# Kernel tuning notes

Hardware: AMD Instinct MI355X
Metric: run time of the kernel (lower is better)

Reference implementation:

```python
import jax, jax.numpy as jnp
import numpy as np

EMB = 64  # hardcoded char embedding / LSTMCell input size in the module


def lstm_cell(x, h, c, Wih, Whh, bih, bhh):
    # torch LSTMCell: gates = x @ Wih.T + bih + h @ Whh.T + bhh, order i,f,g,o
    g = x @ Wih.T + bih + h @ Whh.T + bhh
    i, f, gg, o = jnp.split(g, 4, axis=-1)
    c_new = jax.nn.sigmoid(f) * c + jax.nn.sigmoid(i) * jnp.tanh(gg)
    h_new = jax.nn.sigmoid(o) * jnp.tanh(c_new)
    return h_new, c_new


def setup_inputs() -> dict:
    key = jax.random.key(0)
    ks = jax.random.split(key, 12)
    B, T = 4096, 32
    V, H, O = 256, 512, 64
    s_e = 1.0 / np.sqrt(H)
    inp = {
        "x": jax.random.randint(ks[0], (B, T), 0, V),
        "mask": jnp.ones((B, T), jnp.float32),
        "emb": jax.random.normal(ks[1], (V, EMB), jnp.float32),
        "Wih1": jax.random.uniform(ks[2], (4 * H, EMB), jnp.float32, -s_e, s_e),
        "Whh1": jax.random.uniform(ks[3], (4 * H, H), jnp.float32, -s_e, s_e),
        "bih1": jax.random.uniform(ks[4], (4 * H,), jnp.float32, -s_e, s_e),
        "bhh1": jax.random.uniform(ks[5], (4 * H,), jnp.float32, -s_e, s_e),
        "Wih2": jax.random.uniform(ks[6], (4 * H, EMB), jnp.float32, -s_e, s_e),
        "Whh2": jax.random.uniform(ks[7], (4 * H, H), jnp.float32, -s_e, s_e),
        "bih2": jax.random.uniform(ks[8], (4 * H,), jnp.float32, -s_e, s_e),
        "bhh2": jax.random.uniform(ks[9], (4 * H,), jnp.float32, -s_e, s_e),
        "Wlin": jax.random.uniform(ks[10], (O, 2 * H), jnp.float32, -s_e, s_e),
        "blin": jax.random.uniform(ks[11], (O,), jnp.float32, -s_e, s_e),
    }
    return inp


def reference(x, mask, emb, Wih1, Whh1, bih1, bhh1, Wih2, Whh2, bih2, bhh2, Wlin, blin):
    B, T = x.shape
    H = Whh1.shape[1]
    xe = emb[x].transpose(1, 0, 2)  # [T, B, 64]
    # mask is transposed in the original but never applied; preserved here.

    def step(carry, xs):
        h1, c1, h2, c2 = carry
        x_fwd, x_bwd = xs
        h1, c1 = lstm_cell(x_fwd, h1, c1, Wih1, Whh1, bih1, bhh1)
        h2, c2 = lstm_cell(x_bwd, h2, c2, Wih2, Whh2, bih2, bhh2)
        return (h1, c1, h2, c2), None

    z = jnp.zeros((B, H), xe.dtype)
    (h1, _, h2, _), _ = jax.lax.scan(step, (z, z, z, z), (xe, xe[::-1]))
    # original's transpose/cat/view/transpose is equivalent to feature concat
    h = jnp.concatenate([h1, h2], axis=1)  # [B, 2H]
    return jax.nn.softmax(h @ Wlin.T + blin, axis=1)
```

## Files before the change

### kernel.cpp

```cpp
#include <hip/hip_runtime.h>


typedef __bf16 bf16x8 __attribute__((ext_vector_type(8)));
typedef float  f32x4  __attribute__((ext_vector_type(4)));

constexpr int BATCH = 4096;
constexpr int TSEQ  = 32;
constexpr int HID   = 512;
constexpr int NG    = 2048;
constexpr int VOC   = 256;
constexpr int OUTD  = 64;
constexpr int HBUF  = 64 * BATCH * 8;

__device__ __forceinline__ unsigned short f2bf(float x) {
  unsigned int u = __builtin_bit_cast(unsigned int, x);
  u += 0x7FFFu + ((u >> 16) & 1u);
  return (unsigned short)(u >> 16);
}
__device__ __forceinline__ float bf2f(unsigned short b) {
  unsigned int u = ((unsigned int)b) << 16;
  return __builtin_bit_cast(float, u);
}
__device__ __forceinline__ float fsig(float x) {
  return __fdividef(1.0f, 1.0f + __expf(-x));
}
__device__ __forceinline__ float ftanh(float x) {
  float e = __expf(-2.0f * fabsf(x));
  float t = (1.0f - e) * __fdividef(1.0f, 1.0f + e);
  return copysignf(t, x);
}
__device__ __forceinline__ bf16x8 ld_frag(const unsigned short* p) {
  uint4 v = *(const uint4*)p;
  return __builtin_bit_cast(bf16x8, v);
}
__device__ __forceinline__ void gll16(const void* g, const void* l) {
  __builtin_amdgcn_global_load_lds(
      (const __attribute__((address_space(1))) unsigned int*)g,
      (__attribute__((address_space(3))) unsigned int*)l, 16, 0, 0);
}

__global__ __launch_bounds__(128)
void build_G(const float* __restrict__ emb, const float* __restrict__ Wih,
             const float* __restrict__ bih, const float* __restrict__ bhh,
             float* __restrict__ G) {
  __shared__ float e[64];
  const int v = blockIdx.y;
  const int tid = threadIdx.x;
  if (tid < 64) e[tid] = emb[v * 64 + tid];
  __syncthreads();
  const int n = blockIdx.x * 128 + tid;
  const float4* w4 = (const float4*)&Wih[n * 64];
  float s = bih[n] + bhh[n];
#pragma unroll
  for (int k = 0; k < 16; ++k) {
    float4 wv = w4[k];
    s += wv.x * e[4 * k] + wv.y * e[4 * k + 1] + wv.z * e[4 * k + 2] + wv.w * e[4 * k + 3];
  }
  G[v * NG + n] = s;
}

__global__ __launch_bounds__(256)
void packW(const float* __restrict__ W, unsigned short* __restrict__ hi,
           unsigned short* __restrict__ lo, int kdim, int nch, int total) {
  int p = blockIdx.x * 256 + threadIdx.x;
  if (p >= total) return;
  int lane = p & 63;
  int c = (p >> 6) % nch;
  int f = (p >> 6) / nch;
  int n = f * 16 + (lane & 15);
  int k = c * 32 + (lane >> 4) * 8;
  const float* src = &W[(size_t)n * kdim + k];
  unsigned short* dh = &hi[(size_t)p * 8];
  unsigned short* dl = &lo[(size_t)p * 8];
#pragma unroll
  for (int e = 0; e < 8; ++e) {
    float x = src[e];
    unsigned short h = f2bf(x);
    dh[e] = h;
    dl[e] = f2bf(x - bf2f(h));
  }
}

__global__ __launch_bounds__(256, 4)
void lstm_step(const int* __restrict__ xTok,
               const unsigned short* __restrict__ h1r_hi, const unsigned short* __restrict__ h1r_lo,
               unsigned short* __restrict__ h1w_hi, unsigned short* __restrict__ h1w_lo,
               const unsigned short* __restrict__ h2r_hi, const unsigned short* __restrict__ h2r_lo,
               unsigned short* __restrict__ h2w_hi, unsigned short* __restrict__ h2w_lo,
               float* __restrict__ c1, float* __restrict__ c2,
               const unsigned short* __restrict__ W1_hi, const unsigned short* __restrict__ W1_lo,
               const unsigned short* __restrict__ W2_hi, const unsigned short* __restrict__ W2_lo,
               const float* __restrict__ G1, const float* __restrict__ G2,
               int t) {
  const int tid = threadIdx.x;
  const int bid = blockIdx.x;
  const int cell = (bid >> 2) & 1;
  const int j0   = (((bid & 3) << 1) | ((bid >> 9) & 1)) * 64;
  const int m0   = ((bid >> 3) & 63) * 64;

  const unsigned short* hr_hi = cell ? h2r_hi : h1r_hi;
  const unsigned short* hr_lo = cell ? h2r_lo : h1r_lo;
  unsigned short* hw_hi = cell ? h2w_hi : h1w_hi;
  unsigned short* hw_lo = cell ? h2w_lo : h1w_lo;
  float* cbuf = cell ? c2 : c1;
  const unsigned short* Whi = cell ? W2_hi : W1_hi;
  const unsigned short* Wlo = cell ? W2_lo : W1_lo;
  const float* G = cell ? G2 : G1;
  const int tx = cell ? (TSEQ - 1 - t) : t;

  __shared__ unsigned short ldsA[2][2][8][64][8];
  __shared__ int toks[64];
  if (tid < 64) toks[tid] = xTok[(m0 + tid) * TSEQ + tx];

  const int srow = tid & 63, schk = tid >> 6;
  const unsigned short* ghi = hr_hi + (size_t)schk * 32768 + (size_t)(m0 + srow) * 8;
  const unsigned short* glo = hr_lo + (size_t)schk * 32768 + (size_t)(m0 + srow) * 8;
  char* lbase = ((char*)ldsA) + tid * 16;

  auto stage = [&](int kt, int buf) {
    const size_t go = (size_t)kt * (8 * 32768);
    char* lb = lbase + buf * 16384;
    gll16(ghi + go,             lb);
    gll16(ghi + go + 4 * 32768, lb + 4096);
    gll16(glo + go,             lb + 8192);
    gll16(glo + go + 4 * 32768, lb + 12288);
  };

  stage(0, 0);
  __syncthreads();

  const int lane = tid & 63, hs = tid >> 6;
  const int lg = lane >> 4, ll = lane & 15;

  const int fb = (j0 >> 4) + hs;
  const unsigned short* Bh = Whi + ((size_t)(fb * 16) * 64 + lane) * 8;
  const unsigned short* Bl = Wlo + ((size_t)(fb * 16) * 64 + lane) * 8;

  f32x4 acc[4][4] = {};

#pragma unroll 1
  for (int kt = 0; kt < 8; ++kt) {
    const int cur = kt & 1;
    if (kt < 7) stage(kt + 1, cur ^ 1);
#pragma unroll
    for (int h = 0; h < 2; ++h) {
      const int c = kt * 2 + h;
      bf16x8 bh[4], bl[4];
#pragma unroll
      for (int g = 0; g < 4; ++g) {
        size_t off = ((size_t)(g * 512 + c)) * 512;
        bh[g] = ld_frag(Bh + off);
        bl[g] = ld_frag(Bl + off);
      }
#pragma unroll
      for (int mf = 0; mf < 4; ++mf) {
        const int row = mf * 16 + ll;
        bf16x8 ah = ld_frag(&ldsA[cur][0][h * 4 + lg][row][0]);
        bf16x8 al = ld_frag(&ldsA[cur][1][h * 4 + lg][row][0]);
#pragma unroll
        for (int g = 0; g < 4; ++g) {
          acc[mf][g] = __builtin_amdgcn_mfma_f32_16x16x32_bf16(ah, bh[g], acc[mf][g], 0, 0, 0);
          acc[mf][g] = __builtin_amdgcn_mfma_f32_16x16x32_bf16(al, bh[g], acc[mf][g], 0, 0, 0);
          acc[mf][g] = __builtin_amdgcn_mfma_f32_16x16x32_bf16(ah, bl[g], acc[mf][g], 0, 0, 0);
        }
      }
    }
    __syncthreads();
  }

  const int jcol = j0 + hs * 16 + ll;
#pragma unroll
  for (int mf = 0; mf < 4; ++mf) {
#pragma unroll
    for (int r = 0; r < 4; ++r) {
      int row = mf * 16 + lg * 4 + r;
      int b = m0 + row;
      const float* g4 = &G[(size_t)toks[row] * NG + jcol];
      float pi = acc[mf][0][r] + g4[0];
      float pf = acc[mf][1][r] + g4[512];
      float pg = acc[mf][2][r] + g4[1024];
      float po = acc[mf][3][r] + g4[1536];
      float ig = fsig(pi), fg = fsig(pf), gg = ftanh(pg), og = fsig(po);
      float cold = cbuf[b * HID + jcol];
      float cn = fg * cold + ig * gg;
      cbuf[b * HID + jcol] = cn;
      float hn = og * ftanh(cn);
      unsigned short hh = f2bf(hn);
      unsigned short hl = f2bf(hn - bf2f(hh));
      int hidx = (jcol >> 3) * (BATCH * 8) + b * 8 + (jcol & 7);
      hw_hi[hidx] = hh;
      hw_lo[hidx] = hl;
    }
  }
}

__global__ __launch_bounds__(256)
void final_linsoft(const unsigned short* __restrict__ h1_hi, const unsigned short* __restrict__ h1_lo,
                   const unsigned short* __restrict__ h2_hi, const unsigned short* __restrict__ h2_lo,
                   const unsigned short* __restrict__ WL_hi, const unsigned short* __restrict__ WL_lo,
                   const float* __restrict__ blin, float* __restrict__ out) {
  const int tid = threadIdx.x;
  const int lane = tid & 63;
  const int w = tid >> 6;
  const int lg = lane >> 4, ll = lane & 15;
  const int m0 = blockIdx.x * 64;
  const int arow = m0 + w * 16 + ll;

  f32x4 acc[4] = {};
#pragma unroll 1
  for (int kt = 0; kt < 32; ++kt) {
    const int k0 = kt * 32;
    const unsigned short* ah_ = (k0 < 512) ? h1_hi : h2_hi;
    const unsigned short* al_ = (k0 < 512) ? h1_lo : h2_lo;
    const int kk0 = k0 & 511;
    const int aidx = (kk0 / 8 + lg) * (BATCH * 8) + arow * 8;
    bf16x8 ah = ld_frag(&ah_[aidx]);
    bf16x8 al = ld_frag(&al_[aidx]);
#pragma unroll
    for (int nf = 0; nf < 4; ++nf) {
      size_t boff = (((size_t)nf * 32 + kt) * 64 + lane) * 8;
      bf16x8 bh = ld_frag(&WL_hi[boff]);
      bf16x8 bl = ld_frag(&WL_lo[boff]);
      acc[nf] = __builtin_amdgcn_mfma_f32_16x16x32_bf16(ah, bh, acc[nf], 0, 0, 0);
      acc[nf] = __builtin_amdgcn_mfma_f32_16x16x32_bf16(al, bh, acc[nf], 0, 0, 0);
      acc[nf] = __builtin_amdgcn_mfma_f32_16x16x32_bf16(ah, bl, acc[nf], 0, 0, 0);
    }
  }

  float bl4[4];
#pragma unroll
  for (int nf = 0; nf < 4; ++nf) bl4[nf] = blin[nf * 16 + ll];

#pragma unroll
  for (int r = 0; r < 4; ++r) {
    float z[4];
    float mx = -3.4e38f;
#pragma unroll
    for (int nf = 0; nf < 4; ++nf) { z[nf] = acc[nf][r] + bl4[nf]; mx = fmaxf(mx, z[nf]); }
#pragma unroll
    for (int d = 1; d < 16; d <<= 1) mx = fmaxf(mx, __shfl_xor(mx, d));
    float s = 0.f;
#pragma unroll
    for (int nf = 0; nf < 4; ++nf) { z[nf] = __expf(z[nf] - mx); s += z[nf]; }
#pragma unroll
    for (int d = 1; d < 16; d <<= 1) s += __shfl_xor(s, d);
    float inv = __fdividef(1.0f, s);
    int row = m0 + w * 16 + lg * 4 + r;
#pragma unroll
    for (int nf = 0; nf < 4; ++nf) out[row * OUTD + nf * 16 + ll] = z[nf] * inv;
  }
}

extern "C" void kernel_launch(void* const* d_in, const int* in_sizes, int n_in,
                              void* d_out, int out_size, void* d_ws, size_t ws_size,
                              hipStream_t stream) {
  const int*   x    = (const int*)  d_in[0];
  const float* emb  = (const float*)d_in[2];
  const float* Wih1 = (const float*)d_in[3];
  const float* Whh1 = (const float*)d_in[4];
  const float* bih1 = (const float*)d_in[5];
  const float* bhh1 = (const float*)d_in[6];
  const float* Wih2 = (const float*)d_in[7];
  const float* Whh2 = (const float*)d_in[8];
  const float* bih2 = (const float*)d_in[9];
  const float* bhh2 = (const float*)d_in[10];
  const float* Wlin = (const float*)d_in[11];
  const float* blin = (const float*)d_in[12];
  float* out = (float*)d_out;

  char* p = (char*)d_ws;
  auto alloc = [&](size_t b) { char* r = p; p += (b + 255) & ~(size_t)255; return r; };

  float* G1 = (float*)alloc((size_t)VOC * NG * 4);
  float* G2 = (float*)alloc((size_t)VOC * NG * 4);
  unsigned short* W1_hi = (unsigned short*)alloc((size_t)NG * HID * 2);
  unsigned short* W1_lo = (unsigned short*)alloc((size_t)NG * HID * 2);
  unsigned short* W2_hi = (unsigned short*)alloc((size_t)NG * HID * 2);
  unsigned short* W2_lo = (unsigned short*)alloc((size_t)NG * HID * 2);
  unsigned short* WL_hi = (unsigned short*)alloc((size_t)OUTD * 1024 * 2);
  unsigned short* WL_lo = (unsigned short*)alloc((size_t)OUTD * 1024 * 2);
  unsigned short* h1_hi = (unsigned short*)alloc((size_t)2 * HBUF * 2);
  unsigned short* h1_lo = (unsigned short*)alloc((size_t)2 * HBUF * 2);
  unsigned short* h2_hi = (unsigned short*)alloc((size_t)2 * HBUF * 2);
  unsigned short* h2_lo = (unsigned short*)alloc((size_t)2 * HBUF * 2);
  float* c1 = (float*)alloc((size_t)BATCH * HID * 4);
  float* c2 = (float*)alloc((size_t)BATCH * HID * 4);

  if ((size_t)(p - (char*)d_ws) > ws_size) return;

  hipMemsetAsync(h1_hi, 0, (size_t)HBUF * 2, stream);
  hipMemsetAsync(h1_lo, 0, (size_t)HBUF * 2, stream);
  hipMemsetAsync(h2_hi, 0, (size_t)HBUF * 2, stream);
  hipMemsetAsync(h2_lo, 0, (size_t)HBUF * 2, stream);
  hipMemsetAsync(c1, 0, (size_t)BATCH * HID * 4, stream);
  hipMemsetAsync(c2, 0, (size_t)BATCH * HID * 4, stream);

  packW<<<dim3(512), 256, 0, stream>>>(Whh1, W1_hi, W1_lo, HID, 16, NG * HID / 8);
  packW<<<dim3(512), 256, 0, stream>>>(Whh2, W2_hi, W2_lo, HID, 16, NG * HID / 8);
  packW<<<dim3(32), 256, 0, stream>>>(Wlin, WL_hi, WL_lo, 1024, 32, OUTD * 1024 / 8);
  build_G<<<dim3(16, VOC), 128, 0, stream>>>(emb, Wih1, bih1, bhh1, G1);
  build_G<<<dim3(16, VOC), 128, 0, stream>>>(emb, Wih2, bih2, bhh2, G2);

  for (int t = 0; t < TSEQ; ++t) {
    int rb = t & 1, wb = rb ^ 1;
    lstm_step<<<dim3(1024), 256, 0, stream>>>(x,
        h1_hi + (size_t)rb * HBUF, h1_lo + (size_t)rb * HBUF,
        h1_hi + (size_t)wb * HBUF, h1_lo + (size_t)wb * HBUF,
        h2_hi + (size_t)rb * HBUF, h2_lo + (size_t)rb * HBUF,
        h2_hi + (size_t)wb * HBUF, h2_lo + (size_t)wb * HBUF,
        c1, c2, W1_hi, W1_lo, W2_hi, W2_lo, G1, G2, t);
  }
  final_linsoft<<<dim3(64), 256, 0, stream>>>(h1_hi, h1_lo, h2_hi, h2_lo,
                                              WL_hi, WL_lo, blin, out);
}
```

Baseline: 1.994 ms.

## Switch LSTM step GEMM to 32x32x16 MFMA with repacked recurrent weights

The recurrent-weight GEMM in each LSTM step now uses 32x32x16 bf16 MFMA instructions instead of 16x16x32. Waves are rearranged into a 2x2 grid of 32-row by 32-column tiles, and a new packing kernel lays out Whh in the matching fragment order. The aim is fewer instructions and better operand reuse per MFMA. s_setprio is also raised around the MFMA bursts to favour issuing them. The epilogue is remapped to the 32x32 accumulator layout, and the larger tile shape changes register pressure and per-wave work.

```diff
diff --git a/kernel.cpp b/kernel.cpp
--- a/kernel.cpp
+++ b/kernel.cpp
@@ -3,6 +3,7 @@
 
 typedef __bf16 bf16x8 __attribute__((ext_vector_type(8)));
 typedef float  f32x4  __attribute__((ext_vector_type(4)));
+typedef float  f32x16 __attribute__((ext_vector_type(16)));
 
 constexpr int BATCH = 4096;
 constexpr int TSEQ  = 32;
@@ -70,6 +71,28 @@
   int n = f * 16 + (lane & 15);
   int k = c * 32 + (lane >> 4) * 8;
   const float* src = &W[(size_t)n * kdim + k];
+  unsigned short* dh = &hi[(size_t)p * 8];
+  unsigned short* dl = &lo[(size_t)p * 8];
+#pragma unroll
+  for (int e = 0; e < 8; ++e) {
+    float x = src[e];
+    unsigned short h = f2bf(x);
+    dh[e] = h;
+    dl[e] = f2bf(x - bf2f(h));
+  }
+}
+
+__global__ __launch_bounds__(256)
+void packW32(const float* __restrict__ W, unsigned short* __restrict__ hi,
+             unsigned short* __restrict__ lo, int total) {
+  int p = blockIdx.x * 256 + threadIdx.x;
+  if (p >= total) return;
+  int lane = p & 63;
+  int kc = (p >> 6) & 31;
+  int f  = (p >> 6) >> 5;
+  int n = f * 32 + (lane & 31);
+  int k = kc * 16 + (lane >> 5) * 8;
+  const float* src = &W[(size_t)n * HID + k];
   unsigned short* dh = &hi[(size_t)p * 8];
   unsigned short* dl = &lo[(size_t)p * 8];
 #pragma unroll
@@ -129,68 +152,66 @@
   stage(0, 0);
   __syncthreads();
 
-  const int lane = tid & 63, hs = tid >> 6;
-  const int lg = lane >> 4, ll = lane & 15;
-
-  const int fb = (j0 >> 4) + hs;
-  const unsigned short* Bh = Whi + ((size_t)(fb * 16) * 64 + lane) * 8;
-  const unsigned short* Bl = Wlo + ((size_t)(fb * 16) * 64 + lane) * 8;
-
-  f32x4 acc[4][4] = {};
+  const int lane = tid & 63, wave = tid >> 6;
+  const int mh = wave >> 1, jh = wave & 1;
+  const int l31 = lane & 31, hi5 = lane >> 5;
+
+  size_t bbase[4];
+#pragma unroll
+  for (int g = 0; g < 4; ++g)
+    bbase[g] = ((size_t)(g * 16 + (j0 >> 5) + jh)) * 16384 + (size_t)lane * 8;
+
+  f32x16 acc[4] = {};
 
 #pragma unroll 1
   for (int kt = 0; kt < 8; ++kt) {
     const int cur = kt & 1;
     if (kt < 7) stage(kt + 1, cur ^ 1);
 #pragma unroll
-    for (int h = 0; h < 2; ++h) {
-      const int c = kt * 2 + h;
+    for (int q = 0; q < 4; ++q) {
+      const int kc = kt * 4 + q;
       bf16x8 bh[4], bl[4];
 #pragma unroll
       for (int g = 0; g < 4; ++g) {
-        size_t off = ((size_t)(g * 512 + c)) * 512;
-        bh[g] = ld_frag(Bh + off);
-        bl[g] = ld_frag(Bl + off);
+        size_t off = bbase[g] + (size_t)kc * 512;
+        bh[g] = ld_frag(Whi + off);
+        bl[g] = ld_frag(Wlo + off);
       }
-#pragma unroll
-      for (int mf = 0; mf < 4; ++mf) {
-        const int row = mf * 16 + ll;
-        bf16x8 ah = ld_frag(&ldsA[cur][0][h * 4 + lg][row][0]);
-        bf16x8 al = ld_frag(&ldsA[cur][1][h * 4 + lg][row][0]);
-#pragma unroll
-        for (int g = 0; g < 4; ++g) {
-          acc[mf][g] = __builtin_amdgcn_mfma_f32_16x16x32_bf16(ah, bh[g], acc[mf][g], 0, 0, 0);
-          acc[mf][g] = __builtin_amdgcn_mfma_f32_16x16x32_bf16(al, bh[g], acc[mf][g], 0, 0, 0);
-          acc[mf][g] = __builtin_amdgcn_mfma_f32_16x16x32_bf16(ah, bl[g], acc[mf][g], 0, 0, 0);
-        }
+      bf16x8 ah = ld_frag(&ldsA[cur][0][2 * q + hi5][mh * 32 + l31][0]);
+      bf16x8 al = ld_frag(&ldsA[cur][1][2 * q + hi5][mh * 32 + l31][0]);
+      __builtin_amdgcn_s_setprio(1);
+#pragma unroll
+      for (int g = 0; g < 4; ++g) {
+        acc[g] = __builtin_amdgcn_mfma_f32_32x32x16_bf16(ah, bh[g], acc[g], 0, 0, 0);
+        acc[g] = __builtin_amdgcn_mfma_f32_32x32x16_bf16(al, bh[g], acc[g], 0, 0, 0);
+        acc[g] = __builtin_amdgcn_mfma_f32_32x32x16_bf16(ah, bl[g], acc[g], 0, 0, 0);
       }
+      __builtin_amdgcn_s_setprio(0);
     }
     __syncthreads();
   }
 
-  const int jcol = j0 + hs * 16 + ll;
-#pragma unroll
-  for (int mf = 0; mf < 4; ++mf) {
-#pragma unroll
-    for (int r = 0; r < 4; ++r) {
-      int row = mf * 16 + lg * 4 + r;
-      int b = m0 + row;
-      const float* g4 = &G[(size_t)toks[row] * NG + jcol];
-      float pi = acc[mf][0][r] + g4[0];
-      float pf = acc[mf][1][r] + g4[512];
-      float pg = acc[mf][2][r] + g4[1024];
-      float po = acc[mf][3][r] + g4[1536];
-      float ig = fsig(pi), fg = fsig(pf), gg = ftanh(pg), og = fsig(po);
-      float cold = cbuf[b * HID + jcol];
-      float cn = fg * cold + ig * gg;
-      cbuf[b * HID + jcol] = cn;
-      float hn = og * ftanh(cn);
-      unsigned short hh = f2bf(hn);
-      unsigned short hl = f2bf(hn - bf2f(hh));
-      int hidx = (jcol >> 3) * (BATCH * 8) + b * 8 + (jcol & 7);
-      hw_hi[hidx] = hh;
-      hw_lo[hidx] = hl;
-    }
+  const int jcol = j0 + jh * 32 + l31;
+#pragma unroll
+  for (int r = 0; r < 16; ++r) {
+    const int rowf = (r & 3) + 8 * (r >> 2) + 4 * hi5;
+    const int row = mh * 32 + rowf;
+    const int b = m0 + row;
+    const float* g4 = &G[(size_t)toks[row] * NG + jcol];
+    float pi = acc[0][r] + g4[0];
+    float pf = acc[1][r] + g4[512];
+    float pg = acc[2][r] + g4[1024];
+    float po = acc[3][r] + g4[1536];
+    float ig = fsig(pi), fg = fsig(pf), gg = ftanh(pg), og = fsig(po);
+    float cold = cbuf[b * HID + jcol];
+    float cn = fg * cold + ig * gg;
+    cbuf[b * HID + jcol] = cn;
+    float hn = og * ftanh(cn);
+    unsigned short hh = f2bf(hn);
+    unsigned short hl = f2bf(hn - bf2f(hh));
+    int hidx = (jcol >> 3) * (BATCH * 8) + b * 8 + (jcol & 7);
+    hw_hi[hidx] = hh;
+    hw_lo[hidx] = hl;
   }
 }
 
@@ -295,8 +316,8 @@
   hipMemsetAsync(c1, 0, (size_t)BATCH * HID * 4, stream);
   hipMemsetAsync(c2, 0, (size_t)BATCH * HID * 4, stream);
 
-  packW<<<dim3(512), 256, 0, stream>>>(Whh1, W1_hi, W1_lo, HID, 16, NG * HID / 8);
-  packW<<<dim3(512), 256, 0, stream>>>(Whh2, W2_hi, W2_lo, HID, 16, NG * HID / 8);
+  packW32<<<dim3(512), 256, 0, stream>>>(Whh1, W1_hi, W1_lo, NG * HID / 8);
+  packW32<<<dim3(512), 256, 0, stream>>>(Whh2, W2_hi, W2_lo, NG * HID / 8);
   packW<<<dim3(32), 256, 0, stream>>>(Wlin, WL_hi, WL_lo, 1024, 32, OUTD * 1024 / 8);
   build_G<<<dim3(16, VOC), 128, 0, stream>>>(emb, Wih1, bih1, bhh1, G1);
   build_G<<<dim3(16, VOC), 128, 0, stream>>>(emb, Wih2, bih2, bhh2, G2);
```

Measured after the change: 3.968 ms. +99.0%, slower.

## Deepen LDS staging to a 4-slot ring with prefetch distance two

Applied to the files above, without the earlier changes.

The recurrent GEMM's A-tile staging moves from two large double-buffered stages to sixteen smaller stages in a 4-slot LDS ring, prefetched two steps ahead. B fragments and A fragments are loaded before the MFMA block. MFMA issue priority is raised with setprio, and sched_barriers pin the instruction order. The full __syncthreads is replaced by a bare s_barrier, which may drop the memory-wait and fence semantics the async global-to-LDS loads rely on.

```diff
diff --git a/kernel.cpp b/kernel.cpp
--- a/kernel.cpp
+++ b/kernel.cpp
@@ -108,25 +108,25 @@
   const float* G = cell ? G2 : G1;
   const int tx = cell ? (TSEQ - 1 - t) : t;
 
-  __shared__ unsigned short ldsA[2][2][8][64][8];
+  __shared__ unsigned short ldsA[4][2][4][64][8];
   __shared__ int toks[64];
-  if (tid < 64) toks[tid] = xTok[(m0 + tid) * TSEQ + tx];
-
-  const int srow = tid & 63, schk = tid >> 6;
+
+  toks[tid & 63] = xTok[(size_t)(m0 + (tid & 63)) * TSEQ + tx];
+
+  const int srow = tid & 63, schk = (tid >> 6) & 3;
   const unsigned short* ghi = hr_hi + (size_t)schk * 32768 + (size_t)(m0 + srow) * 8;
   const unsigned short* glo = hr_lo + (size_t)schk * 32768 + (size_t)(m0 + srow) * 8;
-  char* lbase = ((char*)ldsA) + tid * 16;
-
-  auto stage = [&](int kt, int buf) {
-    const size_t go = (size_t)kt * (8 * 32768);
-    char* lb = lbase + buf * 16384;
-    gll16(ghi + go,             lb);
-    gll16(ghi + go + 4 * 32768, lb + 4096);
-    gll16(glo + go,             lb + 8192);
-    gll16(glo + go + 4 * 32768, lb + 12288);
+  char* lb0 = ((char*)ldsA) + (tid >> 6) * 1024 + (tid & 63) * 16;
+
+  auto stage = [&](int s) {
+    char* lb = lb0 + (s & 3) * 8192;
+    const size_t go = (size_t)s * 131072;
+    gll16(ghi + go, lb);
+    gll16(glo + go, lb + 4096);
   };
 
-  stage(0, 0);
+  stage(0);
+  stage(1);
   __syncthreads();
 
   const int lane = tid & 63, hs = tid >> 6;
@@ -139,33 +139,37 @@
   f32x4 acc[4][4] = {};
 
 #pragma unroll 1
-  for (int kt = 0; kt < 8; ++kt) {
-    const int cur = kt & 1;
-    if (kt < 7) stage(kt + 1, cur ^ 1);
-#pragma unroll
-    for (int h = 0; h < 2; ++h) {
-      const int c = kt * 2 + h;
-      bf16x8 bh[4], bl[4];
+  for (int s = 0; s < 16; ++s) {
+    const int cur = s & 3;
+    bf16x8 bh[4], bl[4];
+#pragma unroll
+    for (int g = 0; g < 4; ++g) {
+      size_t off = (size_t)(g * 512 + s) * 512;
+      bh[g] = ld_frag(Bh + off);
+      bl[g] = ld_frag(Bl + off);
+    }
+    __builtin_amdgcn_sched_barrier(0x7);
+    if (s < 14) stage(s + 2);
+    bf16x8 ah[4], al[4];
+#pragma unroll
+    for (int mf = 0; mf < 4; ++mf) {
+      ah[mf] = ld_frag(&ldsA[cur][0][lg][mf * 16 + ll][0]);
+      al[mf] = ld_frag(&ldsA[cur][1][lg][mf * 16 + ll][0]);
+    }
+    __builtin_amdgcn_s_setprio(1);
+#pragma unroll
+    for (int mf = 0; mf < 4; ++mf) {
 #pragma unroll
       for (int g = 0; g < 4; ++g) {
-        size_t off = ((size_t)(g * 512 + c)) * 512;
-        bh[g] = ld_frag(Bh + off);
-        bl[g] = ld_frag(Bl + off);
+        acc[mf][g] = __builtin_amdgcn_mfma_f32_16x16x32_bf16(ah[mf], bh[g], acc[mf][g], 0, 0, 0);
+        acc[mf][g] = __builtin_amdgcn_mfma_f32_16x16x32_bf16(al[mf], bh[g], acc[mf][g], 0, 0, 0);
+        acc[mf][g] = __builtin_amdgcn_mfma_f32_16x16x32_bf16(ah[mf], bl[g], acc[mf][g], 0, 0, 0);
       }
-#pragma unroll
-      for (int mf = 0; mf < 4; ++mf) {
-        const int row = mf * 16 + ll;
-        bf16x8 ah = ld_frag(&ldsA[cur][0][h * 4 + lg][row][0]);
-        bf16x8 al = ld_frag(&ldsA[cur][1][h * 4 + lg][row][0]);
-#pragma unroll
-        for (int g = 0; g < 4; ++g) {
-          acc[mf][g] = __builtin_amdgcn_mfma_f32_16x16x32_bf16(ah, bh[g], acc[mf][g], 0, 0, 0);
-          acc[mf][g] = __builtin_amdgcn_mfma_f32_16x16x32_bf16(al, bh[g], acc[mf][g], 0, 0, 0);
-          acc[mf][g] = __builtin_amdgcn_mfma_f32_16x16x32_bf16(ah, bl[g], acc[mf][g], 0, 0, 0);
-        }
-      }
-    }
-    __syncthreads();
+    }
+    __builtin_amdgcn_s_setprio(0);
+    __builtin_amdgcn_sched_barrier(0);
+    __builtin_amdgcn_s_barrier();
+    __builtin_amdgcn_sched_barrier(0);
   }
 
   const int jcol = j0 + hs * 16 + ll;
```

Result: slower. 2.546 ms (+27.7%).
